# Performance work log

Measured on AMD Instinct MI355X. Metric: run time of the kernel, lower is better.

Reference implementation:

```python
import jax, jax.numpy as jnp
import numpy as np

L, B, H, E, V = 64, 2048, 512, 50, 96
PAD = 0  # padding_idx of the char embedding


def setup_inputs() -> dict:
    key = jax.random.key(0)
    ks = jax.random.split(key, 10)
    s = 0.1  # param scale to keep gates in a sane range
    emb = jax.random.normal(ks[0], (V, E), jnp.float32) * s
    emb = emb.at[PAD].set(0.0)  # padding_idx row is zero
    return {
        "input_ids": jax.random.randint(ks[1], (L, B), 0, V),
        "h0": jax.random.normal(ks[2], (1, B, H), jnp.float32) * s,
        "c0": jax.random.normal(ks[3], (1, B, H), jnp.float32) * s,
        "emb": emb,
        "W_ih": jax.random.normal(ks[4], (4 * H, E), jnp.float32) * s,
        "W_hh": jax.random.normal(ks[5], (4 * H, H), jnp.float32) * s,
        "b_ih": jax.random.normal(ks[6], (4 * H,), jnp.float32) * s,
        "b_hh": jax.random.normal(ks[7], (4 * H,), jnp.float32) * s,
        "W_out": jax.random.normal(ks[8], (V, H), jnp.float32) * s,
        "b_out": jax.random.normal(ks[9], (V,), jnp.float32) * s,
    }


def reference(input_ids, h0, c0, emb, W_ih, W_hh, b_ih, b_hh, W_out, b_out):
    # Embedding lookup: (L, B, E)
    x = emb[input_ids]
    # Precompute input-side gate contributions for all steps: (L, B, 4H)
    x_gates = jnp.einsum('lbe,ge->lbg', x, W_ih) + b_ih + b_hh

    def step(carry, xg):
        h, c = carry  # (B, H) each
        gates = xg + h @ W_hh.T  # (B, 4H), PyTorch gate order i, f, g, o
        i, f, g, o = jnp.split(gates, 4, axis=-1)
        c_new = jax.nn.sigmoid(f) * c + jax.nn.sigmoid(i) * jnp.tanh(g)
        h_new = jax.nn.sigmoid(o) * jnp.tanh(c_new)
        return (h_new, c_new), h_new

    (hL, cL), hs = jax.lax.scan(step, (h0[0], c0[0]), x_gates)
    # Output projection on every step's hidden state: (L, B, V)
    scores = jnp.einsum('lbh,vh->lbv', hs, W_out) + b_out
    return scores, hL[None], cL[None]
```

## Files before the change

kernel.cpp:

```cpp
#include <hip/hip_runtime.h>
#include <stdint.h>

#define LSEQ 64
#define BATCH 2048
#define HID 512
#define NG 2048
#define KP 576
#define VOCAB 96
#define BH (BATCH*HID)

typedef unsigned short u16;
typedef __attribute__((ext_vector_type(8))) short short8;
typedef __attribute__((ext_vector_type(4))) float f32x4;

__device__ __forceinline__ u16 f2bf(float f) {
    union { float f; unsigned u; } v; v.f = f;
    return (u16)((v.u + 0x7FFFu + ((v.u >> 16) & 1u)) >> 16);
}
__device__ __forceinline__ float sig_(float x) { return 1.f / (1.f + __expf(-x)); }
__device__ __forceinline__ float th_(float x) {
    x = fminf(fmaxf(x, -30.f), 30.f);
    float e = __expf(2.f * x);
    return (e - 1.f) / (e + 1.f);
}
__device__ __forceinline__ void gld16(const void* g, void* l) {
    __builtin_amdgcn_global_load_lds(
        (const __attribute__((address_space(1))) unsigned int*)g,
        (__attribute__((address_space(3))) unsigned int*)l, 16, 0, 0);
}
#define WAITV(n) asm volatile("s_waitcnt vmcnt(" #n ")" ::: "memory")

__global__ void k_init(const float* __restrict__ h0, u16* __restrict__ hs0,
                       unsigned* __restrict__ flags) {
    int i = blockIdx.x * 256 + threadIdx.x;
    hs0[i] = f2bf(h0[i]);
    if (i < LSEQ * 256) flags[i] = 0;
}

__global__ void k_pack_w(const float* __restrict__ Wih, const float* __restrict__ Whh,
                         const float* __restrict__ bih, const float* __restrict__ bhh,
                         u16* __restrict__ Wp, float* __restrict__ bp) {
    int id = blockIdx.x * 256 + threadIdx.x;
    int n = id / 72, kc = id % 72;
    int j = n >> 2, q = n & 3;
    int src = q * HID + j;
    int k0 = kc * 8;
    unsigned pk[4];
#pragma unroll
    for (int t = 0; t < 4; ++t) {
        int k = k0 + 2 * t;
        float f0 = (k < 512) ? Whh[src * 512 + k] : ((k < 562) ? Wih[src * 50 + k - 512] : 0.f);
        float f1 = (k + 1 < 512) ? Whh[src * 512 + k + 1]
                                 : ((k + 1 < 562) ? Wih[src * 50 + k + 1 - 512] : 0.f);
        pk[t] = (unsigned)f2bf(f0) | ((unsigned)f2bf(f1) << 16);
    }
    *(uint4*)(Wp + (size_t)n * KP + k0) = make_uint4(pk[0], pk[1], pk[2], pk[3]);
    if (kc == 0) bp[n] = bih[src] + bhh[src];
}

__global__ void k_embed(const int* __restrict__ ids, const float* __restrict__ emb,
                        u16* __restrict__ xb) {
    int id = blockIdx.x * 256 + threadIdx.x;
    int row = id >> 3, kc = id & 7;
    int tok = ids[row];
    int k0 = kc * 8;
    unsigned pk[4];
#pragma unroll
    for (int t = 0; t < 4; ++t) {
        int k = k0 + 2 * t;
        unsigned lo = (k < 50) ? (unsigned)f2bf(emb[tok * 50 + k]) : 0u;
        unsigned hi = (k + 1 < 50) ? (unsigned)f2bf(emb[tok * 50 + k + 1]) : 0u;
        pk[t] = lo | (hi << 16);
    }
    *(uint4*)(xb + (size_t)row * 64 + k0) = make_uint4(pk[0], pk[1], pk[2], pk[3]);
}

__global__ void k_pack_wout(const float* __restrict__ Wo, u16* __restrict__ Wb) {
    int id = blockIdx.x * 256 + threadIdx.x;
    int k0 = id * 8;
    unsigned pk[4];
#pragma unroll
    for (int t = 0; t < 4; ++t)
        pk[t] = (unsigned)f2bf(Wo[k0 + 2 * t]) | ((unsigned)f2bf(Wo[k0 + 2 * t + 1]) << 16);
    *(uint4*)(Wb + k0) = make_uint4(pk[0], pk[1], pk[2], pk[3]);
}

__global__ __launch_bounds__(512, 2) void k_persist(
    const u16* __restrict__ xb, const u16* __restrict__ Wp,
    const float* __restrict__ bp, const float* __restrict__ c0,
    u16* __restrict__ hs, float* __restrict__ foutH, float* __restrict__ foutC,
    unsigned* __restrict__ flags)
{
    __shared__ char smem[57344];
    char* ring = smem;
    u16*  hpk  = (u16*)(smem + 49152);

    const int tid = threadIdx.x;
    const int lane = tid & 63;
    const int w = tid >> 6;
    const int wm = w & 3, wn = w >> 2;
    const int bm = blockIdx.x & 15, bn = blockIdx.x >> 4;
    const int m0 = bm * 128, n0 = bn * 128;
    const int rsub = lane >> 3;
    const int colsw = (((lane & 7) ^ rsub) << 3);
    const int bsub = lane & 15;
    const int usub = lane >> 4;

    short8 wreg[9][2][2];
#pragma unroll
    for (int i = 0; i < 9; ++i) {
        const int koff = (i == 0) ? 512 : (i - 1) * 64;
#pragma unroll
        for (int kk = 0; kk < 2; ++kk)
#pragma unroll
            for (int qm = 0; qm < 2; ++qm)
                wreg[i][kk][qm] = *(const short8*)(
                    Wp + (size_t)(n0 + wm * 32 + qm * 16 + bsub) * KP
                       + koff + kk * 32 + usub * 8);
    }

    float4 bb[2];
#pragma unroll
    for (int qm = 0; qm < 2; ++qm)
        bb[qm] = *(const float4*)(bp + n0 + wm * 32 + qm * 16 + usub * 4);
    float c[2][4];
#pragma unroll
    for (int qm = 0; qm < 2; ++qm)
#pragma unroll
        for (int qn = 0; qn < 4; ++qn)
            c[qm][qn] = c0[(size_t)(m0 + wn * 64 + qn * 16 + bsub) * HID
                           + (n0 >> 2) + wm * 8 + qm * 4 + usub];

#pragma unroll 1
    for (int l = 0; l < LSEQ; ++l) {
        const u16* hsrc = hs + (size_t)l * BH;

        {
            const u16* xs = xb + (size_t)l * BATCH * 64;
#pragma unroll
            for (int it = 0; it < 2; ++it) {
                int wc = w * 2 + it;
                gld16(xs + (size_t)(m0 + wc * 8 + rsub) * 64 + colsw, ring + wc * 1024);
            }
        }
        if (l > 0 && w == 0) {
            const unsigned* f = flags + (unsigned)(l - 1) * 256 + bm * 16;
            for (;;) {
                unsigned v = (lane < 16)
                    ? __hip_atomic_load(f + lane, __ATOMIC_RELAXED, __HIP_MEMORY_SCOPE_AGENT)
                    : 1u;
                if (__all(v != 0)) break;
                __builtin_amdgcn_s_sleep(2);
            }
        }
        __syncthreads();
        __builtin_amdgcn_sched_barrier(0);

#pragma unroll
        for (int it = 0; it < 2; ++it) {
            int wc = w * 2 + it;
            gld16(hsrc + (size_t)(m0 + wc * 8 + rsub) * HID + colsw,
                  ring + 16384 + wc * 1024);
        }

        f32x4 acc[2][4] = {};
#pragma unroll
        for (int i = 0; i < 9; ++i) {
            if (i > 0) {
                if (i < 8) WAITV(2); else WAITV(0);
                __builtin_amdgcn_s_barrier();
                __builtin_amdgcn_sched_barrier(0);
            }
            if (i + 2 <= 8) {
                char* dst = ring + ((i + 2) % 3) * 16384;
#pragma unroll
                for (int it = 0; it < 2; ++it) {
                    int wc = w * 2 + it;
                    gld16(hsrc + (size_t)(m0 + wc * 8 + rsub) * HID + (i + 1) * 64 + colsw,
                          dst + wc * 1024);
                }
            }
            const u16* Bs_ = (const u16*)(ring + (i % 3) * 16384);
#pragma unroll
            for (int kk = 0; kk < 2; ++kk) {
                short8 hv[4];
#pragma unroll
                for (int qn = 0; qn < 4; ++qn)
                    hv[qn] = *(const short8*)(Bs_ + (wn * 64 + qn * 16 + bsub) * 64
                                 + (((kk * 4 + usub) ^ (lane & 7)) << 3));
#pragma unroll
                for (int qm = 0; qm < 2; ++qm)
#pragma unroll
                    for (int qn = 0; qn < 4; ++qn)
                        acc[qm][qn] = __builtin_amdgcn_mfma_f32_16x16x32_bf16(
                            wreg[i][kk][qm], hv[qn], acc[qm][qn], 0, 0, 0);
            }
        }

        const bool last = (l == LSEQ - 1);
#pragma unroll
        for (int qm = 0; qm < 2; ++qm) {
            const float4 b4 = bb[qm];
            const int u_loc = wm * 8 + qm * 4 + usub;
#pragma unroll
            for (int qn = 0; qn < 4; ++qn) {
                const int b_loc = wn * 64 + qn * 16 + bsub;
                float gi = acc[qm][qn][0] + b4.x;
                float gf = acc[qm][qn][1] + b4.y;
                float gg = acc[qm][qn][2] + b4.z;
                float go = acc[qm][qn][3] + b4.w;
                float cn = sig_(gf) * c[qm][qn] + sig_(gi) * th_(gg);
                float hn = sig_(go) * th_(cn);
                c[qm][qn] = cn;
                hpk[b_loc * 32 + (u_loc ^ ((b_loc & 7) << 2))] = f2bf(hn);
                if (last) {
                    size_t ci = (size_t)(m0 + b_loc) * HID + (n0 >> 2) + u_loc;
                    foutH[ci] = hn; foutC[ci] = cn;
                }
            }
        }
        __syncthreads();

        {
            const int b = tid >> 2, seg = tid & 3;
            unsigned long long q[2];
#pragma unroll
            for (int g = 0; g < 2; ++g) {
                int G = seg * 2 + g;
                int gs = G ^ (b & 7);
                q[g] = *(const unsigned long long*)((const char*)hpk + b * 64 + gs * 8);
            }
            u16* dst = hs + (size_t)(l + 1) * BH + (size_t)(m0 + b) * HID
                       + (n0 >> 2) + seg * 8;
            *(uint4*)(dst) = make_uint4((unsigned)q[0], (unsigned)(q[0] >> 32),
                                        (unsigned)q[1], (unsigned)(q[1] >> 32));
        }
        WAITV(0);
        __syncthreads();
        if (tid == 0)
            __hip_atomic_store(flags + (unsigned)l * 256 + bm * 16 + bn, 1u,
                               __ATOMIC_RELAXED, __HIP_MEMORY_SCOPE_AGENT);
    }
}

__global__ __launch_bounds__(256) void k_scores(
    const u16* __restrict__ hsall, const u16* __restrict__ Wb,
    const float* __restrict__ bo, float* __restrict__ out)
{
    __shared__ char smem[28672];
    u16* As = (u16*)smem;
    u16* Bs = (u16*)(smem + 16384);
    const int tid = threadIdx.x, lane = tid & 63, w = tid >> 6;
    const size_t m0 = (size_t)blockIdx.x * 128;
    const int colo = (lane & 7) * 8;
    const int rsub = lane >> 3;
    f32x4 acc[2][6] = {};

    for (int kt = 0; kt < 8; ++kt) {
#pragma unroll
        for (int it = 0; it < 4; ++it) {
            int wc = w * 4 + it;
            int r = wc * 8 + rsub;
            gld16(hsall + (m0 + r) * 512 + kt * 64 + colo, smem + wc * 1024);
        }
#pragma unroll
        for (int it = 0; it < 3; ++it) {
            int wc = w * 3 + it;
            int r = wc * 8 + rsub;
            gld16(Wb + (size_t)r * 512 + kt * 64 + colo, smem + 16384 + wc * 1024);
        }
        __syncthreads();
#pragma unroll
        for (int kk = 0; kk < 2; ++kk) {
            short8 av[2], bv[6];
#pragma unroll
            for (int i = 0; i < 2; ++i)
                av[i] = *(const short8*)(As + (w * 32 + i * 16 + (lane & 15)) * 64 + kk * 32 + (lane >> 4) * 8);
#pragma unroll
            for (int j = 0; j < 6; ++j)
                bv[j] = *(const short8*)(Bs + (j * 16 + (lane & 15)) * 64 + kk * 32 + (lane >> 4) * 8);
#pragma unroll
            for (int i = 0; i < 2; ++i)
#pragma unroll
                for (int j = 0; j < 6; ++j)
                    acc[i][j] = __builtin_amdgcn_mfma_f32_16x16x32_bf16(av[i], bv[j], acc[i][j], 0, 0, 0);
        }
        __syncthreads();
    }
#pragma unroll
    for (int i = 0; i < 2; ++i) {
        int ml = w * 32 + i * 16 + (lane >> 4) * 4;
#pragma unroll
        for (int j = 0; j < 6; ++j) {
            int v = j * 16 + (lane & 15);
            float bbv = bo[v];
#pragma unroll
            for (int r = 0; r < 4; ++r)
                out[(m0 + ml + r) * 96 + v] = acc[i][j][r] + bbv;
        }
    }
}

extern "C" void kernel_launch(void* const* d_in, const int* in_sizes, int n_in,
                              void* d_out, int out_size, void* d_ws, size_t ws_size,
                              hipStream_t stream) {
    const int*   ids  = (const int*)d_in[0];
    const float* h0   = (const float*)d_in[1];
    const float* c0   = (const float*)d_in[2];
    const float* emb  = (const float*)d_in[3];
    const float* Wih  = (const float*)d_in[4];
    const float* Whh  = (const float*)d_in[5];
    const float* bih  = (const float*)d_in[6];
    const float* bhh  = (const float*)d_in[7];
    const float* Wout = (const float*)d_in[8];
    const float* bout = (const float*)d_in[9];

    char* ws = (char*)d_ws;
    u16*      hs    = (u16*)ws;
    unsigned* flags = (unsigned*)(ws + 136314880);
    u16*      xb    = (u16*)(ws + 140509184);
    u16*      Wp    = (u16*)(ws + 157286400);
    float*    bp    = (float*)(ws + 159645696);
    u16*      Wb    = (u16*)(ws + 159653888);
    float*    out   = (float*)d_out;

    k_init<<<dim3(BH / 256), dim3(256), 0, stream>>>(h0, hs, flags);
    k_pack_w<<<dim3(NG * 72 / 256), dim3(256), 0, stream>>>(Wih, Whh, bih, bhh, Wp, bp);
    k_embed<<<dim3(LSEQ * BATCH * 8 / 256), dim3(256), 0, stream>>>(ids, emb, xb);
    k_pack_wout<<<dim3(VOCAB * HID / 8 / 256), dim3(256), 0, stream>>>(Wout, Wb);

    k_persist<<<dim3(256), dim3(512), 0, stream>>>(
        xb, Wp, bp, c0, hs, out + 12582912, out + 12582912 + BH, flags);

    k_scores<<<dim3(LSEQ * BATCH / 128), dim3(256), 0, stream>>>(hs + BH, Wb, bout, out);
}
```

Before: 540.0 us.

## Replace 3-stage K ring with three large LDS slots, fewer barriers per step

The per-timestep K loop of the persistent LSTM kernel used a 3-deep ring of 64-wide K tiles with a barrier before each of 9 tiles. It now uses dynamic LDS (about 152 KB) split into three slots of three tiles each. Most of the h tiles are issued up front, so only 3 barriers and waits are needed per step. This is meant to cut synchronisation and load-latency stalls on the serial recurrence, at the cost of much higher LDS use. With launch_bounds(512,2) that likely leaves one block per CU, and there is an extra hipFuncSetAttribute call on every launch.

```diff
diff --git a/kernel.cpp b/kernel.cpp
--- a/kernel.cpp
+++ b/kernel.cpp
@@ -8,6 +8,10 @@
 #define KP 576
 #define VOCAB 96
 #define BH (BATCH*HID)
+
+#define SLOT(p) ((p) * 49152)
+#define HPK_OFF  147456
+#define SMEM_TOT 155648
 
 typedef unsigned short u16;
 typedef __attribute__((ext_vector_type(8))) short short8;
@@ -91,9 +95,8 @@
     u16* __restrict__ hs, float* __restrict__ foutH, float* __restrict__ foutC,
     unsigned* __restrict__ flags)
 {
-    __shared__ char smem[57344];
-    char* ring = smem;
-    u16*  hpk  = (u16*)(smem + 49152);
+    extern __shared__ char smem[];
+    u16* hpk = (u16*)(smem + HPK_OFF);
 
     const int tid = threadIdx.x;
     const int lane = tid & 63;
@@ -140,7 +143,8 @@
 #pragma unroll
             for (int it = 0; it < 2; ++it) {
                 int wc = w * 2 + it;
-                gld16(xs + (size_t)(m0 + wc * 8 + rsub) * 64 + colsw, ring + wc * 1024);
+                gld16(xs + (size_t)(m0 + wc * 8 + rsub) * 64 + colsw,
+                      smem + SLOT(0) + wc * 1024);
             }
         }
         if (l > 0 && w == 0) {
@@ -157,43 +161,56 @@
         __builtin_amdgcn_sched_barrier(0);
 
 #pragma unroll
-        for (int it = 0; it < 2; ++it) {
-            int wc = w * 2 + it;
-            gld16(hsrc + (size_t)(m0 + wc * 8 + rsub) * HID + colsw,
-                  ring + 16384 + wc * 1024);
-        }
+        for (int t = 0; t < 2; ++t)
+#pragma unroll
+            for (int it = 0; it < 2; ++it) {
+                int wc = w * 2 + it;
+                gld16(hsrc + (size_t)(m0 + wc * 8 + rsub) * HID + t * 64 + colsw,
+                      smem + SLOT(0) + (t + 1) * 16384 + wc * 1024);
+            }
+#pragma unroll
+        for (int t = 0; t < 3; ++t)
+#pragma unroll
+            for (int it = 0; it < 2; ++it) {
+                int wc = w * 2 + it;
+                gld16(hsrc + (size_t)(m0 + wc * 8 + rsub) * HID + (t + 2) * 64 + colsw,
+                      smem + SLOT(1) + t * 16384 + wc * 1024);
+            }
 
         f32x4 acc[2][4] = {};
 #pragma unroll
-        for (int i = 0; i < 9; ++i) {
-            if (i > 0) {
-                if (i < 8) WAITV(2); else WAITV(0);
-                __builtin_amdgcn_s_barrier();
-                __builtin_amdgcn_sched_barrier(0);
-            }
-            if (i + 2 <= 8) {
-                char* dst = ring + ((i + 2) % 3) * 16384;
-#pragma unroll
-                for (int it = 0; it < 2; ++it) {
-                    int wc = w * 2 + it;
-                    gld16(hsrc + (size_t)(m0 + wc * 8 + rsub) * HID + (i + 1) * 64 + colsw,
-                          dst + wc * 1024);
+        for (int p = 0; p < 3; ++p) {
+            if (p < 2) WAITV(6); else WAITV(0);
+            __builtin_amdgcn_s_barrier();
+            __builtin_amdgcn_sched_barrier(0);
+            if (p == 0) {
+#pragma unroll
+                for (int t = 0; t < 3; ++t)
+#pragma unroll
+                    for (int it = 0; it < 2; ++it) {
+                        int wc = w * 2 + it;
+                        gld16(hsrc + (size_t)(m0 + wc * 8 + rsub) * HID + (t + 5) * 64 + colsw,
+                              smem + SLOT(2) + t * 16384 + wc * 1024);
+                    }
+            }
+#pragma unroll
+            for (int t = 0; t < 3; ++t) {
+                const int i = p * 3 + t;
+                const u16* Bs_ = (const u16*)(smem + SLOT(p) + t * 16384);
+#pragma unroll
+                for (int kk = 0; kk < 2; ++kk) {
+                    short8 hv[4];
+#pragma unroll
+                    for (int qn = 0; qn < 4; ++qn)
+                        hv[qn] = *(const short8*)(Bs_ + (wn * 64 + qn * 16 + bsub) * 64
+                                     + (((kk * 4 + usub) ^ (lane & 7)) << 3));
+#pragma unroll
+                    for (int qm = 0; qm < 2; ++qm)
+#pragma unroll
+                        for (int qn = 0; qn < 4; ++qn)
+                            acc[qm][qn] = __builtin_amdgcn_mfma_f32_16x16x32_bf16(
+                                wreg[i][kk][qm], hv[qn], acc[qm][qn], 0, 0, 0);
                 }
-            }
-            const u16* Bs_ = (const u16*)(ring + (i % 3) * 16384);
-#pragma unroll
-            for (int kk = 0; kk < 2; ++kk) {
-                short8 hv[4];
-#pragma unroll
-                for (int qn = 0; qn < 4; ++qn)
-                    hv[qn] = *(const short8*)(Bs_ + (wn * 64 + qn * 16 + bsub) * 64
-                                 + (((kk * 4 + usub) ^ (lane & 7)) << 3));
-#pragma unroll
-                for (int qm = 0; qm < 2; ++qm)
-#pragma unroll
-                    for (int qn = 0; qn < 4; ++qn)
-                        acc[qm][qn] = __builtin_amdgcn_mfma_f32_16x16x32_bf16(
-                            wreg[i][kk][qm], hv[qn], acc[qm][qn], 0, 0, 0);
             }
         }
 
@@ -329,7 +346,9 @@
     k_embed<<<dim3(LSEQ * BATCH * 8 / 256), dim3(256), 0, stream>>>(ids, emb, xb);
     k_pack_wout<<<dim3(VOCAB * HID / 8 / 256), dim3(256), 0, stream>>>(Wout, Wb);
 
-    k_persist<<<dim3(256), dim3(512), 0, stream>>>(
+    hipFuncSetAttribute((const void*)k_persist,
+                        hipFuncAttributeMaxDynamicSharedMemorySize, SMEM_TOT);
+    k_persist<<<dim3(256), dim3(512), SMEM_TOT, stream>>>(
         xb, Wp, bp, c0, hs, out + 12582912, out + 12582912 + BH, flags);
 
     k_scores<<<dim3(LSEQ * BATCH / 128), dim3(256), 0, stream>>>(hs + BH, Wb, bout, out);
```

New measurement: 579.1 us. 7.2% more time.

## Give each wave a private double-buffered LDS ring to drop block barriers

Applied to the files above, without the earlier changes.

Each wave now loads its own 64-row slice of the h/x tiles into a private 16KB double buffer in LDS, instead of sharing a block-wide triple-buffered ring. This removes the per-k-step s_barrier, since a wave only waits on its own vmcnt and lgkmcnt. The cost is that waves sharing the same wn slice each load that tile separately, which multiplies global/L2 traffic. LDS use grows to about 136KB via dynamic shared memory, which likely drops occupancy from 2 blocks per CU to 1.

```diff
diff --git a/kernel.cpp b/kernel.cpp
--- a/kernel.cpp
+++ b/kernel.cpp
@@ -9,6 +9,9 @@
 #define VOCAB 96
 #define BH (BATCH*HID)
 
+#define HPK_OFF  131072
+#define SMEM_TOT 139264
+
 typedef unsigned short u16;
 typedef __attribute__((ext_vector_type(8))) short short8;
 typedef __attribute__((ext_vector_type(4))) float f32x4;
@@ -29,6 +32,7 @@
         (__attribute__((address_space(3))) unsigned int*)l, 16, 0, 0);
 }
 #define WAITV(n) asm volatile("s_waitcnt vmcnt(" #n ")" ::: "memory")
+#define WAITL0() asm volatile("s_waitcnt lgkmcnt(0)" ::: "memory")
 
 __global__ void k_init(const float* __restrict__ h0, u16* __restrict__ hs0,
                        unsigned* __restrict__ flags) {
@@ -91,9 +95,8 @@
     u16* __restrict__ hs, float* __restrict__ foutH, float* __restrict__ foutC,
     unsigned* __restrict__ flags)
 {
-    __shared__ char smem[57344];
-    char* ring = smem;
-    u16*  hpk  = (u16*)(smem + 49152);
+    extern __shared__ char smem[];
+    u16* hpk = (u16*)(smem + HPK_OFF);
 
     const int tid = threadIdx.x;
     const int lane = tid & 63;
@@ -105,6 +108,7 @@
     const int colsw = (((lane & 7) ^ rsub) << 3);
     const int bsub = lane & 15;
     const int usub = lane >> 4;
+    char* ring = smem + w * 16384;
 
     short8 wreg[9][2][2];
 #pragma unroll
@@ -138,10 +142,9 @@
         {
             const u16* xs = xb + (size_t)l * BATCH * 64;
 #pragma unroll
-            for (int it = 0; it < 2; ++it) {
-                int wc = w * 2 + it;
-                gld16(xs + (size_t)(m0 + wc * 8 + rsub) * 64 + colsw, ring + wc * 1024);
-            }
+            for (int cc = 0; cc < 8; ++cc)
+                gld16(xs + (size_t)(m0 + wn * 64 + cc * 8 + rsub) * 64 + colsw,
+                      ring + cc * 1024);
         }
         if (l > 0 && w == 0) {
             const unsigned* f = flags + (unsigned)(l - 1) * 256 + bm * 16;
@@ -157,44 +160,42 @@
         __builtin_amdgcn_sched_barrier(0);
 
 #pragma unroll
-        for (int it = 0; it < 2; ++it) {
-            int wc = w * 2 + it;
-            gld16(hsrc + (size_t)(m0 + wc * 8 + rsub) * HID + colsw,
-                  ring + 16384 + wc * 1024);
-        }
+        for (int cc = 0; cc < 8; ++cc)
+            gld16(hsrc + (size_t)(m0 + wn * 64 + cc * 8 + rsub) * HID + colsw,
+                  ring + 8192 + cc * 1024);
 
         f32x4 acc[2][4] = {};
 #pragma unroll
         for (int i = 0; i < 9; ++i) {
-            if (i > 0) {
-                if (i < 8) WAITV(2); else WAITV(0);
-                __builtin_amdgcn_s_barrier();
-                __builtin_amdgcn_sched_barrier(0);
+            if (i < 8) WAITV(8); else WAITV(0);
+            __builtin_amdgcn_sched_barrier(0);
+            const u16* Bs_ = (const u16*)(ring + (i & 1) * 8192);
+            short8 hv[2][4];
+#pragma unroll
+            for (int kk = 0; kk < 2; ++kk)
+#pragma unroll
+                for (int qn = 0; qn < 4; ++qn)
+                    hv[kk][qn] = *(const short8*)(Bs_ + (qn * 16 + bsub) * 64
+                                     + (((kk * 4 + usub) ^ (bsub & 7)) << 3));
+            WAITL0();
+            __builtin_amdgcn_sched_barrier(0);
+            if (i + 2 <= 8) {
+                char* dst = ring + (i & 1) * 8192;
+#pragma unroll
+                for (int cc = 0; cc < 8; ++cc)
+                    gld16(hsrc + (size_t)(m0 + wn * 64 + cc * 8 + rsub) * HID
+                               + (i + 1) * 64 + colsw,
+                          dst + cc * 1024);
             }
-            if (i + 2 <= 8) {
-                char* dst = ring + ((i + 2) % 3) * 16384;
-#pragma unroll
-                for (int it = 0; it < 2; ++it) {
-                    int wc = w * 2 + it;
-                    gld16(hsrc + (size_t)(m0 + wc * 8 + rsub) * HID + (i + 1) * 64 + colsw,
-                          dst + wc * 1024);
-                }
-            }
-            const u16* Bs_ = (const u16*)(ring + (i % 3) * 16384);
-#pragma unroll
-            for (int kk = 0; kk < 2; ++kk) {
-                short8 hv[4];
-#pragma unroll
-                for (int qn = 0; qn < 4; ++qn)
-                    hv[qn] = *(const short8*)(Bs_ + (wn * 64 + qn * 16 + bsub) * 64
-                                 + (((kk * 4 + usub) ^ (lane & 7)) << 3));
+            __builtin_amdgcn_sched_barrier(0);
+#pragma unroll
+            for (int kk = 0; kk < 2; ++kk)
 #pragma unroll
                 for (int qm = 0; qm < 2; ++qm)
 #pragma unroll
                     for (int qn = 0; qn < 4; ++qn)
                         acc[qm][qn] = __builtin_amdgcn_mfma_f32_16x16x32_bf16(
-                            wreg[i][kk][qm], hv[qn], acc[qm][qn], 0, 0, 0);
-            }
+                            wreg[i][kk][qm], hv[kk][qn], acc[qm][qn], 0, 0, 0);
         }
 
         const bool last = (l == LSEQ - 1);
@@ -329,7 +330,9 @@
     k_embed<<<dim3(LSEQ * BATCH * 8 / 256), dim3(256), 0, stream>>>(ids, emb, xb);
     k_pack_wout<<<dim3(VOCAB * HID / 8 / 256), dim3(256), 0, stream>>>(Wout, Wb);
 
-    k_persist<<<dim3(256), dim3(512), 0, stream>>>(
+    hipFuncSetAttribute((const void*)k_persist,
+                        hipFuncAttributeMaxDynamicSharedMemorySize, SMEM_TOT);
+    k_persist<<<dim3(256), dim3(512), SMEM_TOT, stream>>>(
         xb, Wp, bp, c0, hs, out + 12582912, out + 12582912 + BH, flags);
 
     k_scores<<<dim3(LSEQ * BATCH / 128), dim3(256), 0, stream>>>(hs + BH, Wb, bout, out);
```

Result: slower. 603.2 us (+11.7%).
